# Optimization experiments

Measured on AMD Instinct MI355X. Metric: run time of the kernel, lower is better.

## Reference

```python
import jax, jax.numpy as jnp
import numpy as np

T_FINAL = 1.0
DT_STEP = 0.2
MSQ = 0.1
ALPHA = 0.0
CLIP = 1e8


def dt_to_matrix(dt):
    # dt: (H, W, 3) -> per-pixel 3x3 stencil weights (H, W, 1, 9)
    dt00 = dt
    dt01 = jnp.roll(dt00, 1, axis=1)
    dt10 = jnp.roll(dt00, 1, axis=0)
    dt11 = jnp.roll(dt01, 1, axis=0)
    dt_10 = jnp.roll(dt00, -1, axis=0)
    dt0_1 = jnp.roll(dt00, -1, axis=1)
    dt_1_1 = jnp.roll(dt_10, -1, axis=1)
    dt_11 = jnp.roll(dt_10, 1, axis=1)
    dt1_1 = jnp.roll(dt0_1, 1, axis=0)
    a00, c00, b00 = jnp.split(dt00, 3, axis=-1)
    a01, c01, b01 = jnp.split(dt01, 3, axis=-1)
    a10, c10, b10 = jnp.split(dt10, 3, axis=-1)
    a11, c11, b11 = jnp.split(dt11, 3, axis=-1)
    a0_1, c0_1, b0_1 = jnp.split(dt0_1, 3, axis=-1)
    a_10, c_10, b_10 = jnp.split(dt_10, 3, axis=-1)
    a_1_1, c_1_1, b_1_1 = jnp.split(dt_1_1, 3, axis=-1)
    a_11, c_11, b_11 = jnp.split(dt_11, 3, axis=-1)
    a1_1, c1_1, b1_1 = jnp.split(dt1_1, 3, axis=-1)
    A0 = (jnp.abs(b_11) - b_11 + jnp.abs(b00) - b00) / 4.0
    A1 = (c01 + c00 - jnp.abs(b01) - jnp.abs(b00)) / 2.0
    A2 = (jnp.abs(b11) + b11 + jnp.abs(b00) + b00) / 4.0
    A3 = (a_10 + a00 - jnp.abs(b_10) - jnp.abs(b00)) / 2.0
    A4 = (-(a_10 + 2 * a00 + a10) / 2.0
          - (jnp.abs(b_11) - b_11 + jnp.abs(b11) + b11) / 4.0
          - (jnp.abs(b_1_1) + b_1_1 + jnp.abs(b1_1) - b1_1) / 4.0
          + (jnp.abs(b_10) + jnp.abs(b10) + jnp.abs(b0_1) + jnp.abs(b01) + 2 * jnp.abs(b00)) / 2.0
          - (c0_1 + 2 * c00 + c01) / 2.0)
    A5 = (a10 + a00 - jnp.abs(b10) - jnp.abs(b00)) / 2.0
    A6 = (jnp.abs(b_1_1) + b_1_1 + jnp.abs(b00) + b00) / 4.0
    A7 = (c0_1 + c00 - jnp.abs(b0_1) - jnp.abs(b00)) / 2.0
    A8 = (jnp.abs(b1_1) - b1_1 + jnp.abs(b00) - b00) / 4.0
    return jnp.stack([A0, A1, A2, A3, A4, A5, A6, A7, A8], axis=-1)


def LB(dt, X):
    # per-pixel local 3x3 conv applied independently to each of the N channels
    A = dt_to_matrix(dt)  # (H, W, 1, 9)
    return jax.lax.conv_general_dilated_local(
        X[jnp.newaxis, ...], A, filter_shape=(3, 3), window_strides=(1, 1),
        padding='SAME', dimension_numbers=('CHWN', 'HWOI', 'CHWN'))[0]


def derivative(u):
    # forward finite differences via roll: (2, H, W, N)
    return jnp.stack([jnp.roll(u, -1, axis=0) - u, jnp.roll(u, -1, axis=1) - u])


def nrm(dt, v):
    # quadratic form: a*vx^2 + 2*b*vx*vy + c*vy^2, dt=(H,W,3), v=(2,H,W)
    return dt[:, :, 0] * v[0] ** 2 + 2 * dt[:, :, 2] * (v[1] * v[0]) + dt[:, :, 1] * v[1] ** 2


nrm2 = jax.vmap(nrm, in_axes=[None, -1], out_axes=-1)


def Pi_0(x):
    # projection onto zero-mean (simplex tangent) over channel axis
    return x - jnp.mean(x, axis=-1, keepdims=True)


def setup_inputs() -> dict:
    key = jax.random.key(0)
    k1, k2, k3, k4 = jax.random.split(key, 4)
    H, W, N = 512, 512, 48
    v = jax.random.normal(k1, (H, W, N), dtype=jnp.float32)
    Dt = jax.random.uniform(k2, (H, W, 3), dtype=jnp.float32)
    dg = jax.random.uniform(k3, (H, W, 1), dtype=jnp.float32) * 0.9 + 0.1
    hinv = jax.random.uniform(k4, (H, W, 3), dtype=jnp.float32)
    return {"v": v, "Dt": Dt, "dg": dg, "hinv": hinv}


def reference(v, Dt, dg, hinv):
    n_steps = int(T_FINAL / DT_STEP)  # 5 unrolled Euler steps

    def rhs(x):
        logp = jax.nn.log_softmax(x, axis=-1)
        val = LB(Dt, x) / dg + (1.0 - ALPHA) / 2.0 * nrm2(hinv, derivative(logp)) + MSQ * x
        return jnp.clip(Pi_0(val), -CLIP, CLIP)

    x = v
    for _ in range(n_steps):
        x = x + DT_STEP * rhs(x)
    return x
```

## Files before the change

### kernel.cpp

```cpp
#include <hip/hip_runtime.h>
#include <math.h>

#define HH 512
#define WW 512
#define NCH 48
#define HWPIX (HH * WW)

#define TW 16
#define TH 8
#define HW_HALO 18
#define HH_HALO 10
#define NHALO (HW_HALO * HH_HALO)
#define PSTRIDE 13
#define ASTRIDE 12

__global__ __launch_bounds__(256) void compute_A_kernel(
    const float* __restrict__ Dt, const float* __restrict__ dg,
    float* __restrict__ A) {
  int pix = blockIdx.x * blockDim.x + threadIdx.x;
  int h = pix >> 9;
  int w = pix & (WW - 1);
  int hm = (h == 0) ? HH - 1 : h - 1;
  int hp = (h == HH - 1) ? 0 : h + 1;
  int wm = (w == 0) ? WW - 1 : w - 1;
  int wp = (w == WW - 1) ? 0 : w + 1;

  float aC, cC, bC, cL, bL, cR, bR, aU, bU, aD, bD;
  float bUL, bUR, bDL, bDR;
  {
    int p;
    p = (h * WW + w) * 3;   aC = Dt[p]; cC = Dt[p + 1]; bC = Dt[p + 2];
    p = (h * WW + wm) * 3;  cL = Dt[p + 1]; bL = Dt[p + 2];
    p = (h * WW + wp) * 3;  cR = Dt[p + 1]; bR = Dt[p + 2];
    p = (hm * WW + w) * 3;  aU = Dt[p]; bU = Dt[p + 2];
    p = (hp * WW + w) * 3;  aD = Dt[p]; bD = Dt[p + 2];
    p = (hm * WW + wm) * 3; bUL = Dt[p + 2];
    p = (hm * WW + wp) * 3; bUR = Dt[p + 2];
    p = (hp * WW + wm) * 3; bDL = Dt[p + 2];
    p = (hp * WW + wp) * 3; bDR = Dt[p + 2];
  }

  float A0 = (fabsf(bDL) - bDL + fabsf(bC) - bC) * 0.25f;
  float A1 = (cL + cC - fabsf(bL) - fabsf(bC)) * 0.5f;
  float A2 = (fabsf(bUL) + bUL + fabsf(bC) + bC) * 0.25f;
  float A3 = (aD + aC - fabsf(bD) - fabsf(bC)) * 0.5f;
  float A4 = -(aD + 2.f * aC + aU) * 0.5f
             - (fabsf(bDL) - bDL + fabsf(bUL) + bUL) * 0.25f
             - (fabsf(bDR) + bDR + fabsf(bUR) - bUR) * 0.25f
             + (fabsf(bD) + fabsf(bU) + fabsf(bR) + fabsf(bL) + 2.f * fabsf(bC)) * 0.5f
             - (cR + 2.f * cC + cL) * 0.5f;
  float A5 = (aU + aC - fabsf(bU) - fabsf(bC)) * 0.5f;
  float A6 = (fabsf(bDR) + bDR + fabsf(bC) + bC) * 0.25f;
  float A7 = (cR + cC - fabsf(bR) - fabsf(bC)) * 0.5f;
  float A8 = (fabsf(bUR) - bUR + fabsf(bC) - bC) * 0.25f;

  bool ru = (h > 0), rd = (h < HH - 1), cl = (w > 0), cr = (w < WW - 1);
  if (!(ru && cl)) A0 = 0.f;
  if (!ru)         A1 = 0.f;
  if (!(ru && cr)) A2 = 0.f;
  if (!cl)         A3 = 0.f;
  if (!cr)         A5 = 0.f;
  if (!(rd && cl)) A6 = 0.f;
  if (!rd)         A7 = 0.f;
  if (!(rd && cr)) A8 = 0.f;

  float g = 1.0f / dg[pix];
  float4 o0 = make_float4(A0 * g, A1 * g, A2 * g, A3 * g);
  float4 o1 = make_float4(A4 * g + 0.1f, A5 * g, A6 * g, A7 * g);
  float4 o2 = make_float4(A8 * g, 0.f, 0.f, 0.f);
  float4* Ao = (float4*)A + (size_t)pix * 3;
  Ao[0] = o0;
  Ao[1] = o1;
  Ao[2] = o2;
}

__global__ __launch_bounds__(256, 4) void step_fused_kernel(
    const float* __restrict__ x, const float* __restrict__ A,
    const float* __restrict__ hinv, float* __restrict__ xn) {
  __shared__ float4 tile[NHALO * PSTRIDE];
  __shared__ float lse_s[NHALO];

  int b = blockIdx.x;
  int tile_id = (b & 7) * 256 + (b >> 3);
  int th0 = (tile_id >> 5) * TH;
  int tw0 = (tile_id & 31) * TW;

  int t = threadIdx.x;
  int sub = t & 3;
  int pair = t >> 2;
  int pr = pair >> 3;
  int pc0 = (pair & 7) * 2;
  int pix0 = (th0 + pr) * WW + (tw0 + pc0);
  int pix1 = pix0 + 1;

  float4 v[12];
  bool stager = (t < NHALO);
  if (stager) {
    int r = t / HW_HALO;
    int c = t - r * HW_HALO;
    int gh = (th0 + r - 1) & (HH - 1);
    int gw = (tw0 + c - 1) & (WW - 1);
    const float4* src = (const float4*)x + (size_t)(gh * WW + gw) * 12;
#pragma unroll
    for (int i = 0; i < 12; i++) v[i] = src[i];
  }

  const float4* ap0 = (const float4*)A + (size_t)pix0 * 3;
  const float4* ap1 = (const float4*)A + (size_t)pix1 * 3;
  float4 wA0 = ap0[0], wB0 = ap0[1], wC0 = ap0[2];
  float4 wA1 = ap1[0], wB1 = ap1[1], wC1 = ap1[2];
  const float2* hp = (const float2*)(hinv + (size_t)pix0 * 3);
  float2 h01 = hp[0], h23 = hp[1], h45 = hp[2];

  if (stager) {
    float4 mv = v[0];
#pragma unroll
    for (int i = 1; i < 12; i++) {
      mv.x = fmaxf(mv.x, v[i].x); mv.y = fmaxf(mv.y, v[i].y);
      mv.z = fmaxf(mv.z, v[i].z); mv.w = fmaxf(mv.w, v[i].w);
    }
    float m = fmaxf(fmaxf(mv.x, mv.y), fmaxf(mv.z, mv.w));
    float sx = 0.f, sy = 0.f, sz = 0.f, sw = 0.f;
#pragma unroll
    for (int i = 0; i < 12; i++) {
      sx += __expf(v[i].x - m); sy += __expf(v[i].y - m);
      sz += __expf(v[i].z - m); sw += __expf(v[i].w - m);
      tile[t * PSTRIDE + i] = v[i];
    }
    lse_s[t] = m + __logf((sx + sy) + (sz + sw));
  }
  __syncthreads();

  float wt0[9] = {wA0.x, wA0.y, wA0.z, wA0.w, wB0.x, wB0.y, wB0.z, wB0.w, wC0.x};
  float wt1[9] = {wA1.x, wA1.y, wA1.z, wA1.w, wB1.x, wB1.y, wB1.z, wB1.w, wC1.x};
  float ha0 = h01.x, hc0 = h01.y, hb0 = h23.x;
  float ha1 = h23.y, hc1 = h45.x, hb1 = h45.y;

  int lc0 = (pr + 1) * HW_HALO + (pc0 + 1);
  float l0C = lse_s[lc0];
  float l0R = lse_s[lc0 + 1];
  float l1R = lse_s[lc0 + 2];
  float l0D = lse_s[lc0 + HW_HALO];
  float l1D = lse_s[lc0 + HW_HALO + 1];
  float dld0 = l0C - l0D, dlr0 = l0C - l0R;
  float dld1 = l0R - l1D, dlr1 = l0R - l1R;

  int poff[3][4];
#pragma unroll
  for (int dr = 0; dr < 3; dr++)
#pragma unroll
    for (int dc = 0; dc < 4; dc++)
      poff[dr][dc] = ((pr + dr) * HW_HALO + pc0 + dc) * PSTRIDE;

  float4 vals0[3], vals1[3];
  float sum0 = 0.f, sum1 = 0.f;
#pragma unroll
  for (int j = 0; j < 3; j++) {
    int ch = j * 4 + sub;
    float4 q[3][4];
#pragma unroll
    for (int dr = 0; dr < 3; dr++)
#pragma unroll
      for (int dc = 0; dc < 4; dc++) q[dr][dc] = tile[poff[dr][dc] + ch];

    float4 val0, val1;
#define COMP(f)                                                                \
    {                                                                          \
      float s0_ = wt0[0] * q[0][0].f + wt0[1] * q[0][1].f + wt0[2] * q[0][2].f \
                + wt0[3] * q[1][0].f + wt0[4] * q[1][1].f + wt0[5] * q[1][2].f \
                + wt0[6] * q[2][0].f + wt0[7] * q[2][1].f + wt0[8] * q[2][2].f;\
      float v00 = q[2][1].f - q[1][1].f + dld0;                                \
      float v10 = q[1][2].f - q[1][1].f + dlr0;                                \
      float vv0 = s0_ + 0.5f * (ha0 * v00 * v00 + hc0 * v10 * v10) +           \
                  hb0 * (v00 * v10);                                           \
      val0.f = vv0; sum0 += vv0;                                               \
      float s1_ = wt1[0] * q[0][1].f + wt1[1] * q[0][2].f + wt1[2] * q[0][3].f \
                + wt1[3] * q[1][1].f + wt1[4] * q[1][2].f + wt1[5] * q[1][3].f \
                + wt1[6] * q[2][1].f + wt1[7] * q[2][2].f + wt1[8] * q[2][3].f;\
      float v01 = q[2][2].f - q[1][2].f + dld1;                                \
      float v11 = q[1][3].f - q[1][2].f + dlr1;                                \
      float vv1 = s1_ + 0.5f * (ha1 * v01 * v01 + hc1 * v11 * v11) +           \
                  hb1 * (v01 * v11);                                           \
      val1.f = vv1; sum1 += vv1;                                               \
    }
    COMP(x) COMP(y) COMP(z) COMP(w)
#undef COMP
    vals0[j] = val0;
    vals1[j] = val1;
  }

  sum0 += __shfl_xor(sum0, 1); sum0 += __shfl_xor(sum0, 2);
  sum1 += __shfl_xor(sum1, 1); sum1 += __shfl_xor(sum1, 2);
  float mean0 = sum0 * (1.0f / 48.0f);
  float mean1 = sum1 * (1.0f / 48.0f);

  int cen0 = lc0 * PSTRIDE;
  float4* op0 = (float4*)(xn + (size_t)pix0 * NCH);
  float4* op1 = op0 + 12;
#pragma unroll
  for (int j = 0; j < 3; j++) {
    int ch = j * 4 + sub;
    float4 c0 = tile[cen0 + ch];
    float4 c1 = tile[cen0 + PSTRIDE + ch];
    float4 r0, r1;
    r0.x = c0.x + 0.2f * fminf(fmaxf(vals0[j].x - mean0, -1e8f), 1e8f);
    r0.y = c0.y + 0.2f * fminf(fmaxf(vals0[j].y - mean0, -1e8f), 1e8f);
    r0.z = c0.z + 0.2f * fminf(fmaxf(vals0[j].z - mean0, -1e8f), 1e8f);
    r0.w = c0.w + 0.2f * fminf(fmaxf(vals0[j].w - mean0, -1e8f), 1e8f);
    r1.x = c1.x + 0.2f * fminf(fmaxf(vals1[j].x - mean1, -1e8f), 1e8f);
    r1.y = c1.y + 0.2f * fminf(fmaxf(vals1[j].y - mean1, -1e8f), 1e8f);
    r1.z = c1.z + 0.2f * fminf(fmaxf(vals1[j].z - mean1, -1e8f), 1e8f);
    r1.w = c1.w + 0.2f * fminf(fmaxf(vals1[j].w - mean1, -1e8f), 1e8f);
    op0[ch] = r0;
    op1[ch] = r1;
  }
}

extern "C" void kernel_launch(void* const* d_in, const int* in_sizes, int n_in,
                              void* d_out, int out_size, void* d_ws, size_t ws_size,
                              hipStream_t stream) {
  const float* v    = (const float*)d_in[0];
  const float* Dt   = (const float*)d_in[1];
  const float* dg   = (const float*)d_in[2];
  const float* hinv = (const float*)d_in[3];
  float* out = (float*)d_out;

  float* A    = (float*)d_ws;
  float* xbuf = A + (size_t)ASTRIDE * HWPIX;

  compute_A_kernel<<<dim3(HWPIX / 256), dim3(256), 0, stream>>>(Dt, dg, A);

  const float* cur = v;
  float* nxt = out;
  for (int s = 0; s < 5; s++) {
    step_fused_kernel<<<dim3(HWPIX / 128), dim3(256), 0, stream>>>(cur, A, hinv, nxt);
    if (s == 0) {
      cur = out;
      nxt = xbuf;
    } else {
      float* t = (float*)cur;
      cur = nxt;
      nxt = t;
    }
  }
}
```

Measured before the change: 209.8 us.

## Stage halo tiles via direct global-to-LDS loads and precompute log-sum-exp per step

The halo tile is now staged with the AMD global_load_lds builtin, so data goes straight from global memory into LDS without passing through registers. The layout is per-wave and channel-major with a stride of 65. The per-pixel log-sum-exp is no longer recomputed for every halo pixel in each step. The first kernel computes it for the input, and each step kernel writes it for its own output pixels into a double-buffered array that the next step reads. This removes redundant exp/log work on the halo pixels and the register pressure from staging, at the cost of an extra small global read and write of the LSE array per step and an epilogue reduction.

```diff
diff --git a/kernel.cpp b/kernel.cpp
--- a/kernel.cpp
+++ b/kernel.cpp
@@ -11,12 +11,26 @@
 #define HW_HALO 18
 #define HH_HALO 10
 #define NHALO (HW_HALO * HH_HALO)
-#define PSTRIDE 13
 #define ASTRIDE 12
 
-__global__ __launch_bounds__(256) void compute_A_kernel(
+#define BLK_STRIDE 65
+#define WAVE_STRIDE 780
+
+__device__ __forceinline__ void gl2lds16(const float4* g, float4* l) {
+  __builtin_amdgcn_global_load_lds(
+      (const __attribute__((address_space(1))) void*)g,
+      (__attribute__((address_space(3))) void*)l, 16, 0, 0);
+}
+__device__ __forceinline__ void gl2lds4(const float* g, float* l) {
+  __builtin_amdgcn_global_load_lds(
+      (const __attribute__((address_space(1))) void*)g,
+      (__attribute__((address_space(3))) void*)l, 4, 0, 0);
+}
+
+__global__ __launch_bounds__(256) void compute_A_lse_kernel(
     const float* __restrict__ Dt, const float* __restrict__ dg,
-    float* __restrict__ A) {
+    const float* __restrict__ x, float* __restrict__ A,
+    float* __restrict__ lse0) {
   int pix = blockIdx.x * blockDim.x + threadIdx.x;
   int h = pix >> 9;
   int w = pix & (WW - 1);
@@ -65,20 +79,38 @@
   if (!(rd && cr)) A8 = 0.f;
 
   float g = 1.0f / dg[pix];
-  float4 o0 = make_float4(A0 * g, A1 * g, A2 * g, A3 * g);
-  float4 o1 = make_float4(A4 * g + 0.1f, A5 * g, A6 * g, A7 * g);
-  float4 o2 = make_float4(A8 * g, 0.f, 0.f, 0.f);
   float4* Ao = (float4*)A + (size_t)pix * 3;
-  Ao[0] = o0;
-  Ao[1] = o1;
-  Ao[2] = o2;
+  Ao[0] = make_float4(A0 * g, A1 * g, A2 * g, A3 * g);
+  Ao[1] = make_float4(A4 * g + 0.1f, A5 * g, A6 * g, A7 * g);
+  Ao[2] = make_float4(A8 * g, 0.f, 0.f, 0.f);
+
+  const float4* xv = (const float4*)x + (size_t)pix * 12;
+  float4 u[12];
+#pragma unroll
+  for (int i = 0; i < 12; i++) u[i] = xv[i];
+  float4 mv = u[0];
+#pragma unroll
+  for (int i = 1; i < 12; i++) {
+    mv.x = fmaxf(mv.x, u[i].x); mv.y = fmaxf(mv.y, u[i].y);
+    mv.z = fmaxf(mv.z, u[i].z); mv.w = fmaxf(mv.w, u[i].w);
+  }
+  float m = fmaxf(fmaxf(mv.x, mv.y), fmaxf(mv.z, mv.w));
+  float sx = 0.f, sy = 0.f, sz = 0.f, sw = 0.f;
+#pragma unroll
+  for (int i = 0; i < 12; i++) {
+    sx += __expf(u[i].x - m); sy += __expf(u[i].y - m);
+    sz += __expf(u[i].z - m); sw += __expf(u[i].w - m);
+  }
+  lse0[pix] = m + __logf((sx + sy) + (sz + sw));
 }
 
 __global__ __launch_bounds__(256, 4) void step_fused_kernel(
     const float* __restrict__ x, const float* __restrict__ A,
-    const float* __restrict__ hinv, float* __restrict__ xn) {
-  __shared__ float4 tile[NHALO * PSTRIDE];
-  __shared__ float lse_s[NHALO];
+    const float* __restrict__ hinv, float* __restrict__ xn,
+    const float* __restrict__ lse_in, float* __restrict__ lse_out,
+    int write_lse) {
+  __shared__ float4 tile4[36 * BLK_STRIDE];
+  __shared__ float lse_s[192];
 
   int b = blockIdx.x;
   int tile_id = (b & 7) * 256 + (b >> 3);
@@ -93,16 +125,19 @@
   int pix0 = (th0 + pr) * WW + (tw0 + pc0);
   int pix1 = pix0 + 1;
 
-  float4 v[12];
-  bool stager = (t < NHALO);
-  if (stager) {
+  if (t < NHALO) {
     int r = t / HW_HALO;
     int c = t - r * HW_HALO;
     int gh = (th0 + r - 1) & (HH - 1);
     int gw = (tw0 + c - 1) & (WW - 1);
-    const float4* src = (const float4*)x + (size_t)(gh * WW + gw) * 12;
-#pragma unroll
-    for (int i = 0; i < 12; i++) v[i] = src[i];
+    int gp = gh * WW + gw;
+    const float4* src = (const float4*)x + (size_t)gp * 12;
+    int wv = t >> 6;
+    float4* dst = tile4 + wv * WAVE_STRIDE;
+#pragma unroll
+    for (int i = 0; i < 12; i++)
+      gl2lds16(src + i, dst + i * BLK_STRIDE);
+    gl2lds4(lse_in + gp, lse_s + (wv << 6));
   }
 
   const float4* ap0 = (const float4*)A + (size_t)pix0 * 3;
@@ -112,23 +147,6 @@
   const float2* hp = (const float2*)(hinv + (size_t)pix0 * 3);
   float2 h01 = hp[0], h23 = hp[1], h45 = hp[2];
 
-  if (stager) {
-    float4 mv = v[0];
-#pragma unroll
-    for (int i = 1; i < 12; i++) {
-      mv.x = fmaxf(mv.x, v[i].x); mv.y = fmaxf(mv.y, v[i].y);
-      mv.z = fmaxf(mv.z, v[i].z); mv.w = fmaxf(mv.w, v[i].w);
-    }
-    float m = fmaxf(fmaxf(mv.x, mv.y), fmaxf(mv.z, mv.w));
-    float sx = 0.f, sy = 0.f, sz = 0.f, sw = 0.f;
-#pragma unroll
-    for (int i = 0; i < 12; i++) {
-      sx += __expf(v[i].x - m); sy += __expf(v[i].y - m);
-      sz += __expf(v[i].z - m); sw += __expf(v[i].w - m);
-      tile[t * PSTRIDE + i] = v[i];
-    }
-    lse_s[t] = m + __logf((sx + sy) + (sz + sw));
-  }
   __syncthreads();
 
   float wt0[9] = {wA0.x, wA0.y, wA0.z, wA0.w, wB0.x, wB0.y, wB0.z, wB0.w, wC0.x};
@@ -145,23 +163,26 @@
   float dld0 = l0C - l0D, dlr0 = l0C - l0R;
   float dld1 = l0R - l1D, dlr1 = l0R - l1R;
 
-  int poff[3][4];
+  int base4[3][4];
 #pragma unroll
   for (int dr = 0; dr < 3; dr++)
 #pragma unroll
-    for (int dc = 0; dc < 4; dc++)
-      poff[dr][dc] = ((pr + dr) * HW_HALO + pc0 + dc) * PSTRIDE;
+    for (int dc = 0; dc < 4; dc++) {
+      int p = (pr + dr) * HW_HALO + pc0 + dc;
+      base4[dr][dc] = (p >> 6) * WAVE_STRIDE + (p & 63);
+    }
 
   float4 vals0[3], vals1[3];
   float sum0 = 0.f, sum1 = 0.f;
 #pragma unroll
   for (int j = 0; j < 3; j++) {
     int ch = j * 4 + sub;
+    int choff = ch * BLK_STRIDE;
     float4 q[3][4];
 #pragma unroll
     for (int dr = 0; dr < 3; dr++)
 #pragma unroll
-      for (int dc = 0; dc < 4; dc++) q[dr][dc] = tile[poff[dr][dc] + ch];
+      for (int dc = 0; dc < 4; dc++) q[dr][dc] = tile4[base4[dr][dc] + choff];
 
     float4 val0, val1;
 #define COMP(f)                                                                \
@@ -194,14 +215,18 @@
   float mean0 = sum0 * (1.0f / 48.0f);
   float mean1 = sum1 * (1.0f / 48.0f);
 
-  int cen0 = lc0 * PSTRIDE;
+  int cb0 = (lc0 >> 6) * WAVE_STRIDE + (lc0 & 63);
+  int lc1 = lc0 + 1;
+  int cb1 = (lc1 >> 6) * WAVE_STRIDE + (lc1 & 63);
   float4* op0 = (float4*)(xn + (size_t)pix0 * NCH);
   float4* op1 = op0 + 12;
+  float4 rr0[3], rr1[3];
 #pragma unroll
   for (int j = 0; j < 3; j++) {
     int ch = j * 4 + sub;
-    float4 c0 = tile[cen0 + ch];
-    float4 c1 = tile[cen0 + PSTRIDE + ch];
+    int choff = ch * BLK_STRIDE;
+    float4 c0 = tile4[cb0 + choff];
+    float4 c1 = tile4[cb1 + choff];
     float4 r0, r1;
     r0.x = c0.x + 0.2f * fminf(fmaxf(vals0[j].x - mean0, -1e8f), 1e8f);
     r0.y = c0.y + 0.2f * fminf(fmaxf(vals0[j].y - mean0, -1e8f), 1e8f);
@@ -213,6 +238,38 @@
     r1.w = c1.w + 0.2f * fminf(fmaxf(vals1[j].w - mean1, -1e8f), 1e8f);
     op0[ch] = r0;
     op1[ch] = r1;
+    rr0[j] = r0;
+    rr1[j] = r1;
+  }
+
+  if (write_lse) {
+    float4 m4;
+    m4.x = fmaxf(fmaxf(rr0[0].x, rr0[1].x), rr0[2].x);
+    m4.y = fmaxf(fmaxf(rr0[0].y, rr0[1].y), rr0[2].y);
+    m4.z = fmaxf(fmaxf(rr0[0].z, rr0[1].z), rr0[2].z);
+    m4.w = fmaxf(fmaxf(rr0[0].w, rr0[1].w), rr0[2].w);
+    float m0 = fmaxf(fmaxf(m4.x, m4.y), fmaxf(m4.z, m4.w));
+    m4.x = fmaxf(fmaxf(rr1[0].x, rr1[1].x), rr1[2].x);
+    m4.y = fmaxf(fmaxf(rr1[0].y, rr1[1].y), rr1[2].y);
+    m4.z = fmaxf(fmaxf(rr1[0].z, rr1[1].z), rr1[2].z);
+    m4.w = fmaxf(fmaxf(rr1[0].w, rr1[1].w), rr1[2].w);
+    float m1 = fmaxf(fmaxf(m4.x, m4.y), fmaxf(m4.z, m4.w));
+    m0 = fmaxf(m0, __shfl_xor(m0, 1)); m0 = fmaxf(m0, __shfl_xor(m0, 2));
+    m1 = fmaxf(m1, __shfl_xor(m1, 1)); m1 = fmaxf(m1, __shfl_xor(m1, 2));
+    float s0 = 0.f, s1 = 0.f;
+#pragma unroll
+    for (int j = 0; j < 3; j++) {
+      s0 += __expf(rr0[j].x - m0) + __expf(rr0[j].y - m0) +
+            __expf(rr0[j].z - m0) + __expf(rr0[j].w - m0);
+      s1 += __expf(rr1[j].x - m1) + __expf(rr1[j].y - m1) +
+            __expf(rr1[j].z - m1) + __expf(rr1[j].w - m1);
+    }
+    s0 += __shfl_xor(s0, 1); s0 += __shfl_xor(s0, 2);
+    s1 += __shfl_xor(s1, 1); s1 += __shfl_xor(s1, 2);
+    if (sub == 0) {
+      lse_out[pix0] = m0 + __logf(s0);
+      lse_out[pix1] = m1 + __logf(s1);
+    }
   }
 }
 
@@ -227,13 +284,18 @@
 
   float* A    = (float*)d_ws;
   float* xbuf = A + (size_t)ASTRIDE * HWPIX;
-
-  compute_A_kernel<<<dim3(HWPIX / 256), dim3(256), 0, stream>>>(Dt, dg, A);
+  float* lse0 = xbuf + (size_t)NCH * HWPIX;
+  float* lse1 = lse0 + HWPIX;
+
+  compute_A_lse_kernel<<<dim3(HWPIX / 256), dim3(256), 0, stream>>>(
+      Dt, dg, v, A, lse0);
 
   const float* cur = v;
   float* nxt = out;
+  float* lsebuf[2] = {lse0, lse1};
   for (int s = 0; s < 5; s++) {
-    step_fused_kernel<<<dim3(HWPIX / 128), dim3(256), 0, stream>>>(cur, A, hinv, nxt);
+    step_fused_kernel<<<dim3(HWPIX / 128), dim3(256), 0, stream>>>(
+        cur, A, hinv, nxt, lsebuf[s & 1], lsebuf[(s + 1) & 1], (s < 4) ? 1 : 0);
     if (s == 0) {
       cur = out;
       nxt = xbuf;
```

Result: slower. 250.3 us (+19.3%).
